# Kernel optimization log

Hardware: AMD Instinct MI355X
Metric: run time of the kernel (lower is better)

Reference implementation:

```python
import jax, jax.numpy as jnp
import numpy as np
from jax import lax


def _norm(a):
    a = np.asarray(a, np.float32)
    return a / (np.sqrt((a ** 2).sum()) + 1e-12)


LO = {
    'db4': _norm([-0.0105974017850021, 0.0328830116668852, 0.0308413818355607, -0.1870348117188811,
                  -0.0279837694169839, 0.6308807679295904, 0.7148465705529155, 0.2303778133088964]),
    'db6': _norm([0.00107730108499558, -0.00477725751101065, -0.0005538422009938, 0.03158203931748603,
                  0.02752286553030533, -0.0975016055873225, -0.12976686756709563, 0.22626469396544,
                  0.3152503517092432, -0.7511339080210959, 0.4946238903984534, 0.1115407433501095]),
    'sym6': _norm([-0.007800708325034148, 0.001767711864242804, 0.04472490177066578, -0.02106029251230056,
                   -0.0726375227866, 0.3379294217282401, 0.787641141030194, 0.4910559419267466,
                   -0.048311742585632, -0.1179901111484105, 0.00349071208421747, 0.01540410932702737]),
    'coif5': _norm([-3.459977283621256e-05, -7.098330313814114e-05, 0.0004662169601128863, 0.001117518770890601,
                    -0.002574517688750223, -0.00900797613666158, 0.015880544863615904, 0.03455502757306163,
                    -0.08230192710688598, -0.07179982161931202, 0.42848347637761874, 0.7937772226256206,
                    0.4051769024096169, -0.06112339000267287, -0.06577191128185562, 0.023452696141836267,
                    0.007782596427325418, -0.003793512864491014, -0.0002606761356811993, 0.000107502882505652,
                    1.10319778524429e-05, -5.520763127949e-06, -1.0682196848076e-06, 5.236425333584e-07,
                    1.125098976034e-07, -5.417490769329e-08, -8.8631e-09, 4.2921e-09, 6.7e-10, -3.2e-10]),
}
FIR_NAMES = ['db4', 'db6', 'sym6', 'coif5']
LIFT97 = (-1.586134342, -0.05298011854, 0.8829110762, 0.4435068522)


def _neighbor_sum(y):
    # 0.5*(y[i-1]+y[i+1]) with reflect padding on last axis
    yp = jnp.pad(y, [(0, 0)] * (y.ndim - 1) + [(1, 1)], mode='reflect')
    return 0.5 * (yp[..., :-2] + yp[..., 2:])


def _lift(xf, steps, sA, sD):
    # xf: [N, C]; even/odd split along signal axis, then predict/update lifting steps
    even, odd = xf[:, 0::2], xf[:, 1::2]
    for coeff, is_predict in steps:
        if is_predict:
            odd = odd + coeff * _neighbor_sum(even)
        else:
            even = even + coeff * _neighbor_sum(odd)
    return sA * even, sD * odd


def _fir(xf, lo_np):
    # xf: [N, C]; QMF analysis pair, reflect-padded 'same-ish' correlation (Lout = C-2 for even L)
    L = lo_np.shape[0]
    n = np.arange(L)
    hi_np = ((-1.0) ** n).astype(np.float32) * lo_np[::-1]
    pad = (L - 1) // 2
    pl, pr = (pad - 1, pad) if L % 2 == 0 else (pad, pad)
    xp = jnp.pad(xf[:, None, :], ((0, 0), (0, 0), (pl, pr)), mode='reflect')
    rhs = jnp.asarray(np.stack([lo_np, hi_np])[:, None, :])  # [2,1,L]
    out = lax.conv_general_dilated(xp, rhs, (1,), 'VALID', dimension_numbers=('NCH', 'OIH', 'NCH'))
    return out[:, 0], out[:, 1]


def _resize_linear(x, out_size):
    # matches torch F.interpolate(mode='linear', align_corners=False) on last axis
    Lin = x.shape[-1]
    if Lin == out_size:
        return x
    src = (np.arange(out_size) + 0.5) * (Lin / out_size) - 0.5
    src = np.clip(src, 0.0, None)
    i0 = np.minimum(np.floor(src).astype(np.int32), Lin - 1)
    i1 = np.minimum(i0 + 1, Lin - 1)
    w = jnp.asarray((src - i0).astype(np.float32))
    return x[..., i0] * (1.0 - w) + x[..., i1] * w


def setup_inputs() -> dict:
    key = jax.random.key(0)
    ks = jax.random.split(key, 4)
    B, C, H, W, O, K = 8, 64, 128, 128, 64, 6
    G = max(4, int(C * 0.25))
    return {
        'x': jax.random.normal(ks[0], (B, C, H, W), jnp.float32),
        'gate_w1': jax.random.normal(ks[1], (G, C), jnp.float32) * 0.1,
        'gate_b1': jnp.zeros((G,), jnp.float32),
        'gate_w2': jax.random.normal(ks[2], (K, G), jnp.float32) * 0.1,
        'gate_b2': jnp.zeros((K,), jnp.float32),
        'proj_w': jax.random.normal(ks[3], (O, 2 * C), jnp.float32) * 0.05,
        'proj_b': jnp.zeros((O,), jnp.float32),
        'scale53_A': jnp.asarray(1.0, jnp.float32),
        'scale53_D': jnp.asarray(1.0, jnp.float32),
        'scale97_A': jnp.asarray(1.149604398, jnp.float32),
        'scale97_D': jnp.asarray(1.0 / 1.149604398, jnp.float32),
    }


def reference(x, gate_w1, gate_b1, gate_w2, gate_b2, proj_w, proj_b,
              scale53_A, scale53_D, scale97_A, scale97_D):
    B, C, H, W = x.shape
    # per-pixel gate over K candidates (two 1x1 convs + softmax)
    h = jax.nn.relu(jnp.einsum('bchw,gc->bghw', x, gate_w1) + gate_b1[None, :, None, None])
    logits = jnp.einsum('bghw,kg->bkhw', h, gate_w2) + gate_b2[None, :, None, None]
    gate = jax.nn.softmax(logits, axis=1)

    xf = x.transpose(0, 2, 3, 1).reshape(B * H * W, C)  # signal axis = channels
    As, Ds = [], []
    for name in FIR_NAMES:
        A, D = _fir(xf, LO[name])
        As.append(_resize_linear(A, C))
        Ds.append(_resize_linear(D, C))
    A, D = _lift(xf, [(-0.5, True), (0.25, False)], scale53_A, scale53_D)
    As.append(_resize_linear(A, C)); Ds.append(_resize_linear(D, C))
    al, be, ga, de = LIFT97
    A, D = _lift(xf, [(al, True), (be, False), (ga, True), (de, False)], scale97_A, scale97_D)
    As.append(_resize_linear(A, C)); Ds.append(_resize_linear(D, C))

    A_cat = jnp.stack(As, axis=1)  # [BHW, K, C]
    D_cat = jnp.stack(Ds, axis=1)
    wm = gate.transpose(0, 2, 3, 1).reshape(B * H * W, -1)
    wm = wm / (wm.sum(axis=1, keepdims=True) + 1e-12)
    A_f = jnp.einsum('nkc,nk->nc', A_cat, wm)
    D_f = jnp.einsum('nkc,nk->nc', D_cat, wm)

    Y = jnp.concatenate([A_f, D_f], axis=1).reshape(B, H, W, 2 * C)
    out = jnp.einsum('bhwc,oc->bohw', Y, proj_w) + proj_b[None, :, None, None]
    return out
```

## Files before the change

### kernel.cpp

```cpp
#include <hip/hip_runtime.h>
#include <hip/hip_bf16.h>
#include <math.h>

typedef __bf16 bf16x4 __attribute__((ext_vector_type(4)));
typedef __bf16 bf16x8 __attribute__((ext_vector_type(8)));
typedef float  f32x4  __attribute__((ext_vector_type(4)));

#define HW 16384
#define CCH 64
#define OCH 64

__device__ static const float FIRTAB[62] = {
  -0.0105974017850021f, 0.0328830116668852f, 0.0308413818355607f, -0.1870348117188811f,
  -0.0279837694169839f, 0.6308807679295904f, 0.7148465705529155f, 0.2303778133088964f,
  0.00107730108499558f, -0.00477725751101065f, -0.0005538422009938f, 0.03158203931748603f,
  0.02752286553030533f, -0.0975016055873225f, -0.12976686756709563f, 0.22626469396544f,
  0.3152503517092432f, -0.7511339080210959f, 0.4946238903984534f, 0.1115407433501095f,
  -0.007800708325034148f, 0.001767711864242804f, 0.04472490177066578f, -0.02106029251230056f,
  -0.0726375227866f, 0.3379294217282401f, 0.787641141030194f, 0.4910559419267466f,
  -0.048311742585632f, -0.1179901111484105f, 0.00349071208421747f, 0.01540410932702737f,
  -3.459977283621256e-05f, -7.098330313814114e-05f, 0.0004662169601128863f, 0.001117518770890601f,
  -0.002574517688750223f, -0.00900797613666158f, 0.015880544863615904f, 0.03455502757306163f,
  -0.08230192710688598f, -0.07179982161931202f, 0.42848347637761874f, 0.7937772226256206f,
  0.4051769024096169f, -0.06112339000267287f, -0.06577191128185562f, 0.023452696141836267f,
  0.007782596427325418f, -0.003793512864491014f, -0.0002606761356811993f, 0.000107502882505652f,
  1.10319778524429e-05f, -5.520763127949e-06f, -1.0682196848076e-06f, 5.236425333584e-07f,
  1.125098976034e-07f, -5.417490769329e-08f, -8.8631e-09f, 4.2921e-09f, 6.7e-10f, -3.2e-10f
};
__device__ static const int FIR_OFF[4] = {0, 8, 20, 32};
__device__ static const int FIR_LEN[4] = {8, 12, 12, 30};

__global__ __launch_bounds__(256) void setup_P(
    const float* __restrict__ pw,
    const float* __restrict__ s53A, const float* __restrict__ s53D,
    const float* __restrict__ s97A, const float* __restrict__ s97D,
    __bf16* __restrict__ Pout)
{
  __shared__ float tmpA[62][64];
  __shared__ float tmpD[62][64];
  __shared__ float matA[64][64];
  __shared__ float matD[64][64];
  __shared__ float pwld[8][128];
  __shared__ float rawS[32], loS[32], hiS[32];

  const int k = blockIdx.x >> 3;
  const int q = blockIdx.x & 7;
  const int t = threadIdx.x;

  {
    const float* src = pw + q * 8 * 128;
    #pragma unroll
    for (int i = 0; i < 4; ++i)
      ((float*)pwld)[t + i * 256] = src[t + i * 256];
  }

  if (k < 4) {
    const int L = FIR_LEN[k], off = FIR_OFF[k];
    const int pl = (L - 1) / 2 - 1;

    if (t < L) rawS[t] = FIRTAB[off + t];
    __syncthreads();
    float ss = 0.f;
    for (int l = 0; l < L; ++l) { float vv = rawS[l]; ss += vv * vv; }
    const float inv = 1.f / (sqrtf(ss) + 1e-12f);
    if (t < L) {
      loS[t] = rawS[t] * inv;
      hiS[t] = ((t & 1) ? -1.f : 1.f) * rawS[L - 1 - t] * inv;
    }
    __syncthreads();

    for (int e = t; e < 62 * 64; e += 256) {
      const int i = e >> 6, c = e & 63;
      const int base = pl - i;
      const int l1 = c + base;
      const int l2 = -c + base;
      const int l3 = 126 - c + base;
      float va = 0.f, vd = 0.f;
      if (l1 >= 0 && l1 < L)           { va += loS[l1]; vd += hiS[l1]; }
      if (c > 0 && l2 >= 0 && l2 < L)  { va += loS[l2]; vd += hiS[l2]; }
      if (c < 63 && l3 >= 0 && l3 < L) { va += loS[l3]; vd += hiS[l3]; }
      tmpA[i][c] = va; tmpD[i][c] = vd;
    }
    __syncthreads();
  } else {
    for (int e = t; e < 32 * 64; e += 256) {
      const int i = e >> 6, c = e & 63;
      tmpA[i][c] = (c == 2 * i)     ? 1.f : 0.f;
      tmpD[i][c] = (c == 2 * i + 1) ? 1.f : 0.f;
    }
    float cf[4]; int nst;
    if (k == 4) { cf[0] = -0.5f; cf[1] = 0.25f; cf[2] = 0.f; cf[3] = 0.f; nst = 2; }
    else { cf[0] = -1.586134342f; cf[1] = -0.05298011854f;
           cf[2] = 0.8829110762f; cf[3] = 0.4435068522f; nst = 4; }
    __syncthreads();
    for (int s = 0; s < nst; ++s) {
      for (int e = t; e < 32 * 64; e += 256) {
        const int i = e >> 6, c = e & 63;
        const int im = (i == 0) ? 1 : i - 1;
        const int ip = (i == 31) ? 30 : i + 1;
        if ((s & 1) == 0)
          tmpD[i][c] += cf[s] * 0.5f * (tmpA[im][c] + tmpA[ip][c]);
        else
          tmpA[i][c] += cf[s] * 0.5f * (tmpD[im][c] + tmpD[ip][c]);
      }
      __syncthreads();
    }
  }

  {
    const int Lin = (k < 4) ? 62 : 32;
    float sA = 1.f, sD = 1.f;
    if (k == 4) { sA = s53A[0]; sD = s53D[0]; }
    if (k == 5) { sA = s97A[0]; sD = s97D[0]; }
    const float step = (float)Lin / 64.0f;
    for (int e = t; e < 64 * 64; e += 256) {
      const int o = e >> 6, c = e & 63;
      float src = (o + 0.5f) * step - 0.5f;
      src = fmaxf(src, 0.f);
      int i0 = (int)floorf(src); if (i0 > Lin - 1) i0 = Lin - 1;
      int i1 = i0 + 1;           if (i1 > Lin - 1) i1 = Lin - 1;
      float w = src - (float)i0;
      matA[o][c] = sA * ((1.f - w) * tmpA[i0][c] + w * tmpA[i1][c]);
      matD[o][c] = sD * ((1.f - w) * tmpD[i0][c] + w * tmpD[i1][c]);
    }
  }
  __syncthreads();

  {
    const int oo = t >> 5;
    const int o  = q * 8 + oo;
    const int c0 = (t & 31) * 2;
    float acc0 = 0.f, acc1 = 0.f;
    #pragma unroll 8
    for (int j = 0; j < 64; ++j) {
      const float wa = pwld[oo][j];
      const float wd = pwld[oo][64 + j];
      acc0 += wa * matA[j][c0]     + wd * matD[j][c0];
      acc1 += wa * matA[j][c0 + 1] + wd * matD[j][c0 + 1];
    }
    const int mf = o >> 4;
    #pragma unroll
    for (int cc = 0; cc < 2; ++cc) {
      const int c = c0 + cc;
      const int s = k * 2 + (c >> 5);
      const int lane = (o & 15) | (((c & 31) >> 3) << 4);
      const int e = c & 7;
      Pout[(((s * 4 + mf) * 64 + lane) << 3) + e] = (__bf16)(cc ? acc1 : acc0);
    }
  }
}

__global__ __launch_bounds__(256, 2) void wavelet_main(
    const float* __restrict__ xg,
    const float* __restrict__ gw1, const float* __restrict__ gb1,
    const float* __restrict__ gw2, const float* __restrict__ gb2,
    const float* __restrict__ pbias,
    const __bf16* __restrict__ Pws,
    float* __restrict__ outg)
{
  __shared__ __align__(16) unsigned char xt[256 * 128];
  __shared__ __align__(16) float wmld[256 * 8];

  const int t    = threadIdx.x;
  const int w    = t >> 6;
  const int lane = t & 63;
  const int lr   = lane & 15;
  const int kq   = lane >> 4;

  const int blk   = blockIdx.x;
  const int b     = blk >> 6;
  const int pbase = (blk & 63) << 8;

  const int pq  = lane & 15;
  const int cg  = lane >> 4;
  const int px0 = w * 64 + pq * 4;

  const float* s = xg + (size_t)b * (CCH * HW) + (size_t)(cg * 16) * HW + pbase + px0;
  f32x4 v[16];
  #pragma unroll
  for (int r = 0; r < 16; ++r) v[r] = *(const f32x4*)(s + (size_t)r * HW);

  bf16x8 A[12];
  #pragma unroll
  for (int kk = 0; kk < 6; ++kk)
    #pragma unroll
    for (int sh = 0; sh < 2; ++sh)
      A[kk * 2 + sh] = *(const bf16x8*)(Pws + (size_t)((((2 * kk + sh) * 4 + w) * 64 + lane) << 3));

  bf16x8 W1a[2];
  {
    const float* wp = gw1 + lr * 64 + kq * 8;
    #pragma unroll
    for (int hh = 0; hh < 2; ++hh) {
      f32x4 lo = *(const f32x4*)(wp + hh * 32);
      f32x4 hi = *(const f32x4*)(wp + hh * 32 + 4);
      bf16x8 a;
      #pragma unroll
      for (int e = 0; e < 4; ++e) { a[e] = (__bf16)lo[e]; a[e + 4] = (__bf16)hi[e]; }
      W1a[hh] = a;
    }
  }
  const f32x4 gb1v  = *(const f32x4*)(gb1 + kq * 4);
  const f32x4 biasv = *(const f32x4*)(pbias + w * 16 + kq * 4);

  #pragma unroll
  for (int i = 0; i < 4; ++i) {
    const int px = px0 + i;
    bf16x8 w0, w1;
    #pragma unroll
    for (int e = 0; e < 8; ++e) { w0[e] = (__bf16)v[e][i]; w1[e] = (__bf16)v[8 + e][i]; }
    *(bf16x8*)&xt[px * 128 + (((cg * 2)     ^ (px & 7)) << 4)] = w0;
    *(bf16x8*)&xt[px * 128 + (((cg * 2 + 1) ^ (px & 7)) << 4)] = w1;
  }

  #pragma unroll
  for (int pp = 0; pp < 4; ++pp) {
    const int col = (w * 4 + pp) * 16 + lr;
    const bf16x8 B0 = *(const bf16x8*)&xt[col * 128 + ((kq       ^ (col & 7)) << 4)];
    const bf16x8 B1 = *(const bf16x8*)&xt[col * 128 + (((4 + kq) ^ (col & 7)) << 4)];

    f32x4 h = {0.f, 0.f, 0.f, 0.f};
    h = __builtin_amdgcn_mfma_f32_16x16x32_bf16(W1a[0], B0, h, 0, 0, 0);
    h = __builtin_amdgcn_mfma_f32_16x16x32_bf16(W1a[1], B1, h, 0, 0, 0);
    float hr[4];
    #pragma unroll
    for (int j = 0; j < 4; ++j) hr[j] = fmaxf(h[j] + gb1v[j], 0.f);

    float lg[6];
    #pragma unroll
    for (int kk = 0; kk < 6; ++kk) {
      const f32x4 w2 = *(const f32x4*)(gw2 + kk * 16 + kq * 4);
      lg[kk] = w2[0] * hr[0] + w2[1] * hr[1] + w2[2] * hr[2] + w2[3] * hr[3];
    }
    #pragma unroll
    for (int kk = 0; kk < 6; ++kk) lg[kk] += __shfl_xor(lg[kk], 16);
    #pragma unroll
    for (int kk = 0; kk < 6; ++kk) lg[kk] += __shfl_xor(lg[kk], 32);
    #pragma unroll
    for (int kk = 0; kk < 6; ++kk) lg[kk] += gb2[kk];

    float mx = fmaxf(fmaxf(fmaxf(lg[0], lg[1]), fmaxf(lg[2], lg[3])), fmaxf(lg[4], lg[5]));
    float ex[6], ssum = 0.f;
    #pragma unroll
    for (int kk = 0; kk < 6; ++kk) { ex[kk] = __expf(lg[kk] - mx); ssum += ex[kk]; }
    const float sinv = __builtin_amdgcn_rcpf(ssum);
    if (kq == 0) {
      f32x4 o0 = { ex[0] * sinv, ex[1] * sinv, ex[2] * sinv, ex[3] * sinv };
      f32x4 o1 = { ex[4] * sinv, ex[5] * sinv, 0.f, 0.f };
      *(f32x4*)&wmld[col * 8 + 0] = o0;
      *(f32x4*)&wmld[col * 8 + 4] = o1;
    }
  }
  __syncthreads();

  float* outb = outg + (size_t)b * (OCH * HW) + pbase;

  #pragma unroll
  for (int pg = 0; pg < 16; ++pg) {
    const int col = pg * 16 + lr;
    const bf16x8 B0 = *(const bf16x8*)&xt[col * 128 + ((kq       ^ (col & 7)) << 4)];
    const bf16x8 B1 = *(const bf16x8*)&xt[col * 128 + (((4 + kq) ^ (col & 7)) << 4)];
    const f32x4 wv0 = *(const f32x4*)&wmld[col * 8 + 0];
    const f32x4 wv1 = *(const f32x4*)&wmld[col * 8 + 4];
    const float wmv[6] = { wv0[0], wv0[1], wv0[2], wv0[3], wv1[0], wv1[1] };

    f32x4 facc = biasv;
    #pragma unroll
    for (int kk = 0; kk < 6; ++kk) {
      f32x4 y = {0.f, 0.f, 0.f, 0.f};
      y = __builtin_amdgcn_mfma_f32_16x16x32_bf16(A[2 * kk    ], B0, y, 0, 0, 0);
      y = __builtin_amdgcn_mfma_f32_16x16x32_bf16(A[2 * kk + 1], B1, y, 0, 0, 0);
      #pragma unroll
      for (int j = 0; j < 4; ++j) facc[j] += wmv[kk] * y[j];
    }
    #pragma unroll
    for (int j = 0; j < 4; ++j) {
      const int o = w * 16 + kq * 4 + j;
      __builtin_nontemporal_store(facc[j], &outb[(size_t)o * HW + col]);
    }
  }
}

extern "C" void kernel_launch(void* const* d_in, const int* in_sizes, int n_in,
                              void* d_out, int out_size, void* d_ws, size_t ws_size,
                              hipStream_t stream) {
  const float* x    = (const float*)d_in[0];
  const float* gw1  = (const float*)d_in[1];
  const float* gb1  = (const float*)d_in[2];
  const float* gw2  = (const float*)d_in[3];
  const float* gb2  = (const float*)d_in[4];
  const float* pw   = (const float*)d_in[5];
  const float* pb   = (const float*)d_in[6];
  const float* s53A = (const float*)d_in[7];
  const float* s53D = (const float*)d_in[8];
  const float* s97A = (const float*)d_in[9];
  const float* s97D = (const float*)d_in[10];
  __bf16* Pws = (__bf16*)d_ws;
  float* out = (float*)d_out;

  setup_P<<<48, 256, 0, stream>>>(pw, s53A, s53D, s97A, s97D, Pws);
  wavelet_main<<<512, 256, 0, stream>>>(x, gw1, gb1, gw2, gb2, pb, Pws, out);
}
```

Before: 30.79 us.

## Fuse setup and main kernels into one cooperative kernel with grid sync

Merges the projection-matrix setup kernel and the main wavelet kernel into a single cooperative launch. The first 48 blocks build the bf16 projection table after issuing their input loads, then a grid-wide sync publishes it before the projection MFMAs. Shared memory is a union of both stages' buffers. This aims to remove the second launch and the serialization gap between the kernels, and to overlap setup with input loading and the gating computation. In exchange it adds a grid barrier, relies on all 512 blocks being co-resident, and delays 48 blocks with extra work; it falls back to the two-kernel path if the cooperative launch fails.

```diff
diff --git a/kernel.cpp b/kernel.cpp
--- a/kernel.cpp
+++ b/kernel.cpp
@@ -1,6 +1,9 @@
 #include <hip/hip_runtime.h>
 #include <hip/hip_bf16.h>
+#include <hip/hip_cooperative_groups.h>
 #include <math.h>
+
+namespace cg = cooperative_groups;
 
 typedef __bf16 bf16x4 __attribute__((ext_vector_type(4)));
 typedef __bf16 bf16x8 __attribute__((ext_vector_type(8)));
@@ -30,42 +33,46 @@
 __device__ static const int FIR_OFF[4] = {0, 8, 20, 32};
 __device__ static const int FIR_LEN[4] = {8, 12, 12, 30};
 
-__global__ __launch_bounds__(256) void setup_P(
+struct PS {
+  float tmpA[62][64];
+  float tmpD[62][64];
+  float matA[64][64];
+  float matD[64][64];
+  float pwld[8][128];
+  float rawS[32], loS[32], hiS[32];
+};
+struct MS {
+  unsigned char xt[256 * 128];
+  float wmld[256 * 8];
+};
+union SU { PS p; MS m; };
+
+__device__ __forceinline__ void build_P(
+    PS& S, int k, int q, int t,
     const float* __restrict__ pw,
     const float* __restrict__ s53A, const float* __restrict__ s53D,
     const float* __restrict__ s97A, const float* __restrict__ s97D,
     __bf16* __restrict__ Pout)
 {
-  __shared__ float tmpA[62][64];
-  __shared__ float tmpD[62][64];
-  __shared__ float matA[64][64];
-  __shared__ float matD[64][64];
-  __shared__ float pwld[8][128];
-  __shared__ float rawS[32], loS[32], hiS[32];
-
-  const int k = blockIdx.x >> 3;
-  const int q = blockIdx.x & 7;
-  const int t = threadIdx.x;
-
   {
     const float* src = pw + q * 8 * 128;
     #pragma unroll
     for (int i = 0; i < 4; ++i)
-      ((float*)pwld)[t + i * 256] = src[t + i * 256];
+      ((float*)S.pwld)[t + i * 256] = src[t + i * 256];
   }
 
   if (k < 4) {
     const int L = FIR_LEN[k], off = FIR_OFF[k];
     const int pl = (L - 1) / 2 - 1;
 
-    if (t < L) rawS[t] = FIRTAB[off + t];
+    if (t < L) S.rawS[t] = FIRTAB[off + t];
     __syncthreads();
     float ss = 0.f;
-    for (int l = 0; l < L; ++l) { float vv = rawS[l]; ss += vv * vv; }
+    for (int l = 0; l < L; ++l) { float vv = S.rawS[l]; ss += vv * vv; }
     const float inv = 1.f / (sqrtf(ss) + 1e-12f);
     if (t < L) {
-      loS[t] = rawS[t] * inv;
-      hiS[t] = ((t & 1) ? -1.f : 1.f) * rawS[L - 1 - t] * inv;
+      S.loS[t] = S.rawS[t] * inv;
+      S.hiS[t] = ((t & 1) ? -1.f : 1.f) * S.rawS[L - 1 - t] * inv;
     }
     __syncthreads();
 
@@ -76,17 +83,17 @@
       const int l2 = -c + base;
       const int l3 = 126 - c + base;
       float va = 0.f, vd = 0.f;
-      if (l1 >= 0 && l1 < L)           { va += loS[l1]; vd += hiS[l1]; }
-      if (c > 0 && l2 >= 0 && l2 < L)  { va += loS[l2]; vd += hiS[l2]; }
-      if (c < 63 && l3 >= 0 && l3 < L) { va += loS[l3]; vd += hiS[l3]; }
-      tmpA[i][c] = va; tmpD[i][c] = vd;
+      if (l1 >= 0 && l1 < L)           { va += S.loS[l1]; vd += S.hiS[l1]; }
+      if (c > 0 && l2 >= 0 && l2 < L)  { va += S.loS[l2]; vd += S.hiS[l2]; }
+      if (c < 63 && l3 >= 0 && l3 < L) { va += S.loS[l3]; vd += S.hiS[l3]; }
+      S.tmpA[i][c] = va; S.tmpD[i][c] = vd;
     }
     __syncthreads();
   } else {
     for (int e = t; e < 32 * 64; e += 256) {
       const int i = e >> 6, c = e & 63;
-      tmpA[i][c] = (c == 2 * i)     ? 1.f : 0.f;
-      tmpD[i][c] = (c == 2 * i + 1) ? 1.f : 0.f;
+      S.tmpA[i][c] = (c == 2 * i)     ? 1.f : 0.f;
+      S.tmpD[i][c] = (c == 2 * i + 1) ? 1.f : 0.f;
     }
     float cf[4]; int nst;
     if (k == 4) { cf[0] = -0.5f; cf[1] = 0.25f; cf[2] = 0.f; cf[3] = 0.f; nst = 2; }
@@ -99,9 +106,9 @@
         const int im = (i == 0) ? 1 : i - 1;
         const int ip = (i == 31) ? 30 : i + 1;
         if ((s & 1) == 0)
-          tmpD[i][c] += cf[s] * 0.5f * (tmpA[im][c] + tmpA[ip][c]);
+          S.tmpD[i][c] += cf[s] * 0.5f * (S.tmpA[im][c] + S.tmpA[ip][c]);
         else
-          tmpA[i][c] += cf[s] * 0.5f * (tmpD[im][c] + tmpD[ip][c]);
+          S.tmpA[i][c] += cf[s] * 0.5f * (S.tmpD[im][c] + S.tmpD[ip][c]);
       }
       __syncthreads();
     }
@@ -120,8 +127,8 @@
       int i0 = (int)floorf(src); if (i0 > Lin - 1) i0 = Lin - 1;
       int i1 = i0 + 1;           if (i1 > Lin - 1) i1 = Lin - 1;
       float w = src - (float)i0;
-      matA[o][c] = sA * ((1.f - w) * tmpA[i0][c] + w * tmpA[i1][c]);
-      matD[o][c] = sD * ((1.f - w) * tmpD[i0][c] + w * tmpD[i1][c]);
+      S.matA[o][c] = sA * ((1.f - w) * S.tmpA[i0][c] + w * S.tmpA[i1][c]);
+      S.matD[o][c] = sD * ((1.f - w) * S.tmpD[i0][c] + w * S.tmpD[i1][c]);
     }
   }
   __syncthreads();
@@ -133,10 +140,10 @@
     float acc0 = 0.f, acc1 = 0.f;
     #pragma unroll 8
     for (int j = 0; j < 64; ++j) {
-      const float wa = pwld[oo][j];
-      const float wd = pwld[oo][64 + j];
-      acc0 += wa * matA[j][c0]     + wd * matD[j][c0];
-      acc1 += wa * matA[j][c0 + 1] + wd * matD[j][c0 + 1];
+      const float wa = S.pwld[oo][j];
+      const float wd = S.pwld[oo][64 + j];
+      acc0 += wa * S.matA[j][c0]     + wd * S.matD[j][c0];
+      acc1 += wa * S.matA[j][c0 + 1] + wd * S.matD[j][c0 + 1];
     }
     const int mf = o >> 4;
     #pragma unroll
@@ -148,6 +155,154 @@
       Pout[(((s * 4 + mf) * 64 + lane) << 3) + e] = (__bf16)(cc ? acc1 : acc0);
     }
   }
+  __syncthreads();
+}
+
+__global__ __launch_bounds__(256, 2) void fused(
+    const float* __restrict__ xg,
+    const float* __restrict__ gw1, const float* __restrict__ gb1,
+    const float* __restrict__ gw2, const float* __restrict__ gb2,
+    const float* __restrict__ pw,  const float* __restrict__ pbias,
+    const float* __restrict__ s53A, const float* __restrict__ s53D,
+    const float* __restrict__ s97A, const float* __restrict__ s97D,
+    __bf16* __restrict__ Pws,
+    float* __restrict__ outg)
+{
+  __shared__ __align__(16) SU u;
+
+  const int t    = threadIdx.x;
+  const int w    = t >> 6;
+  const int lane = t & 63;
+  const int lr   = lane & 15;
+  const int kq   = lane >> 4;
+
+  const int blk   = blockIdx.x;
+  const int b     = blk >> 6;
+  const int pbase = (blk & 63) << 8;
+
+  const int pq  = lane & 15;
+  const int cg  = lane >> 4;
+  const int px0 = w * 64 + pq * 4;
+
+  const float* s = xg + (size_t)b * (CCH * HW) + (size_t)(cg * 16) * HW + pbase + px0;
+  f32x4 v[16];
+  #pragma unroll
+  for (int r = 0; r < 16; ++r) v[r] = *(const f32x4*)(s + (size_t)r * HW);
+
+  if (blk < 48)
+    build_P(u.p, blk >> 3, blk & 7, t, pw, s53A, s53D, s97A, s97D, Pws);
+
+  bf16x8 W1a[2];
+  {
+    const float* wp = gw1 + lr * 64 + kq * 8;
+    #pragma unroll
+    for (int hh = 0; hh < 2; ++hh) {
+      f32x4 lo = *(const f32x4*)(wp + hh * 32);
+      f32x4 hi = *(const f32x4*)(wp + hh * 32 + 4);
+      bf16x8 a;
+      #pragma unroll
+      for (int e = 0; e < 4; ++e) { a[e] = (__bf16)lo[e]; a[e + 4] = (__bf16)hi[e]; }
+      W1a[hh] = a;
+    }
+  }
+  const f32x4 gb1v  = *(const f32x4*)(gb1 + kq * 4);
+  const f32x4 biasv = *(const f32x4*)(pbias + w * 16 + kq * 4);
+
+  #pragma unroll
+  for (int i = 0; i < 4; ++i) {
+    const int px = px0 + i;
+    bf16x8 w0, w1;
+    #pragma unroll
+    for (int e = 0; e < 8; ++e) { w0[e] = (__bf16)v[e][i]; w1[e] = (__bf16)v[8 + e][i]; }
+    *(bf16x8*)&u.m.xt[px * 128 + (((cg * 2)     ^ (px & 7)) << 4)] = w0;
+    *(bf16x8*)&u.m.xt[px * 128 + (((cg * 2 + 1) ^ (px & 7)) << 4)] = w1;
+  }
+
+  #pragma unroll
+  for (int pp = 0; pp < 4; ++pp) {
+    const int col = (w * 4 + pp) * 16 + lr;
+    const bf16x8 B0 = *(const bf16x8*)&u.m.xt[col * 128 + ((kq       ^ (col & 7)) << 4)];
+    const bf16x8 B1 = *(const bf16x8*)&u.m.xt[col * 128 + (((4 + kq) ^ (col & 7)) << 4)];
+
+    f32x4 h = {0.f, 0.f, 0.f, 0.f};
+    h = __builtin_amdgcn_mfma_f32_16x16x32_bf16(W1a[0], B0, h, 0, 0, 0);
+    h = __builtin_amdgcn_mfma_f32_16x16x32_bf16(W1a[1], B1, h, 0, 0, 0);
+    float hr[4];
+    #pragma unroll
+    for (int j = 0; j < 4; ++j) hr[j] = fmaxf(h[j] + gb1v[j], 0.f);
+
+    float lg[6];
+    #pragma unroll
+    for (int kk = 0; kk < 6; ++kk) {
+      const f32x4 w2 = *(const f32x4*)(gw2 + kk * 16 + kq * 4);
+      lg[kk] = w2[0] * hr[0] + w2[1] * hr[1] + w2[2] * hr[2] + w2[3] * hr[3];
+    }
+    #pragma unroll
+    for (int kk = 0; kk < 6; ++kk) lg[kk] += __shfl_xor(lg[kk], 16);
+    #pragma unroll
+    for (int kk = 0; kk < 6; ++kk) lg[kk] += __shfl_xor(lg[kk], 32);
+    #pragma unroll
+    for (int kk = 0; kk < 6; ++kk) lg[kk] += gb2[kk];
+
+    float mx = fmaxf(fmaxf(fmaxf(lg[0], lg[1]), fmaxf(lg[2], lg[3])), fmaxf(lg[4], lg[5]));
+    float ex[6], ssum = 0.f;
+    #pragma unroll
+    for (int kk = 0; kk < 6; ++kk) { ex[kk] = __expf(lg[kk] - mx); ssum += ex[kk]; }
+    const float sinv = __builtin_amdgcn_rcpf(ssum);
+    if (kq == 0) {
+      f32x4 o0 = { ex[0] * sinv, ex[1] * sinv, ex[2] * sinv, ex[3] * sinv };
+      f32x4 o1 = { ex[4] * sinv, ex[5] * sinv, 0.f, 0.f };
+      *(f32x4*)&u.m.wmld[col * 8 + 0] = o0;
+      *(f32x4*)&u.m.wmld[col * 8 + 4] = o1;
+    }
+  }
+
+  cg::this_grid().sync();
+
+  bf16x8 A[12];
+  #pragma unroll
+  for (int kk = 0; kk < 6; ++kk)
+    #pragma unroll
+    for (int sh = 0; sh < 2; ++sh)
+      A[kk * 2 + sh] = *(const bf16x8*)(Pws + (size_t)((((2 * kk + sh) * 4 + w) * 64 + lane) << 3));
+
+  float* outb = outg + (size_t)b * (OCH * HW) + pbase;
+
+  #pragma unroll
+  for (int pg = 0; pg < 16; ++pg) {
+    const int col = pg * 16 + lr;
+    const bf16x8 B0 = *(const bf16x8*)&u.m.xt[col * 128 + ((kq       ^ (col & 7)) << 4)];
+    const bf16x8 B1 = *(const bf16x8*)&u.m.xt[col * 128 + (((4 + kq) ^ (col & 7)) << 4)];
+    const f32x4 wv0 = *(const f32x4*)&u.m.wmld[col * 8 + 0];
+    const f32x4 wv1 = *(const f32x4*)&u.m.wmld[col * 8 + 4];
+    const float wmv[6] = { wv0[0], wv0[1], wv0[2], wv0[3], wv1[0], wv1[1] };
+
+    f32x4 facc = biasv;
+    #pragma unroll
+    for (int kk = 0; kk < 6; ++kk) {
+      f32x4 y = {0.f, 0.f, 0.f, 0.f};
+      y = __builtin_amdgcn_mfma_f32_16x16x32_bf16(A[2 * kk    ], B0, y, 0, 0, 0);
+      y = __builtin_amdgcn_mfma_f32_16x16x32_bf16(A[2 * kk + 1], B1, y, 0, 0, 0);
+      #pragma unroll
+      for (int j = 0; j < 4; ++j) facc[j] += wmv[kk] * y[j];
+    }
+    #pragma unroll
+    for (int j = 0; j < 4; ++j) {
+      const int o = w * 16 + kq * 4 + j;
+      __builtin_nontemporal_store(facc[j], &outb[(size_t)o * HW + col]);
+    }
+  }
+}
+
+__global__ __launch_bounds__(256) void setup_P(
+    const float* __restrict__ pw,
+    const float* __restrict__ s53A, const float* __restrict__ s53D,
+    const float* __restrict__ s97A, const float* __restrict__ s97D,
+    __bf16* __restrict__ Pout)
+{
+  __shared__ __align__(16) PS S;
+  build_P(S, blockIdx.x >> 3, blockIdx.x & 7, threadIdx.x,
+          pw, s53A, s53D, s97A, s97D, Pout);
 }
 
 __global__ __launch_bounds__(256, 2) void wavelet_main(
@@ -158,8 +313,7 @@
     const __bf16* __restrict__ Pws,
     float* __restrict__ outg)
 {
-  __shared__ __align__(16) unsigned char xt[256 * 128];
-  __shared__ __align__(16) float wmld[256 * 8];
+  __shared__ __align__(16) MS m;
 
   const int t    = threadIdx.x;
   const int w    = t >> 6;
@@ -209,15 +363,15 @@
     bf16x8 w0, w1;
     #pragma unroll
     for (int e = 0; e < 8; ++e) { w0[e] = (__bf16)v[e][i]; w1[e] = (__bf16)v[8 + e][i]; }
-    *(bf16x8*)&xt[px * 128 + (((cg * 2)     ^ (px & 7)) << 4)] = w0;
-    *(bf16x8*)&xt[px * 128 + (((cg * 2 + 1) ^ (px & 7)) << 4)] = w1;
+    *(bf16x8*)&m.xt[px * 128 + (((cg * 2)     ^ (px & 7)) << 4)] = w0;
+    *(bf16x8*)&m.xt[px * 128 + (((cg * 2 + 1) ^ (px & 7)) << 4)] = w1;
   }
 
   #pragma unroll
   for (int pp = 0; pp < 4; ++pp) {
     const int col = (w * 4 + pp) * 16 + lr;
-    const bf16x8 B0 = *(const bf16x8*)&xt[col * 128 + ((kq       ^ (col & 7)) << 4)];
-    const bf16x8 B1 = *(const bf16x8*)&xt[col * 128 + (((4 + kq) ^ (col & 7)) << 4)];
+    const bf16x8 B0 = *(const bf16x8*)&m.xt[col * 128 + ((kq       ^ (col & 7)) << 4)];
+    const bf16x8 B1 = *(const bf16x8*)&m.xt[col * 128 + (((4 + kq) ^ (col & 7)) << 4)];
 
     f32x4 h = {0.f, 0.f, 0.f, 0.f};
     h = __builtin_amdgcn_mfma_f32_16x16x32_bf16(W1a[0], B0, h, 0, 0, 0);
@@ -247,8 +401,8 @@
     if (kq == 0) {
       f32x4 o0 = { ex[0] * sinv, ex[1] * sinv, ex[2] * sinv, ex[3] * sinv };
       f32x4 o1 = { ex[4] * sinv, ex[5] * sinv, 0.f, 0.f };
-      *(f32x4*)&wmld[col * 8 + 0] = o0;
-      *(f32x4*)&wmld[col * 8 + 4] = o1;
+      *(f32x4*)&m.wmld[col * 8 + 0] = o0;
+      *(f32x4*)&m.wmld[col * 8 + 4] = o1;
     }
   }
   __syncthreads();
@@ -258,10 +412,10 @@
   #pragma unroll
   for (int pg = 0; pg < 16; ++pg) {
     const int col = pg * 16 + lr;
-    const bf16x8 B0 = *(const bf16x8*)&xt[col * 128 + ((kq       ^ (col & 7)) << 4)];
-    const bf16x8 B1 = *(const bf16x8*)&xt[col * 128 + (((4 + kq) ^ (col & 7)) << 4)];
-    const f32x4 wv0 = *(const f32x4*)&wmld[col * 8 + 0];
-    const f32x4 wv1 = *(const f32x4*)&wmld[col * 8 + 4];
+    const bf16x8 B0 = *(const bf16x8*)&m.xt[col * 128 + ((kq       ^ (col & 7)) << 4)];
+    const bf16x8 B1 = *(const bf16x8*)&m.xt[col * 128 + (((4 + kq) ^ (col & 7)) << 4)];
+    const f32x4 wv0 = *(const f32x4*)&m.wmld[col * 8 + 0];
+    const f32x4 wv1 = *(const f32x4*)&m.wmld[col * 8 + 4];
     const float wmv[6] = { wv0[0], wv0[1], wv0[2], wv0[3], wv1[0], wv1[1] };
 
     f32x4 facc = biasv;
@@ -298,6 +452,15 @@
   __bf16* Pws = (__bf16*)d_ws;
   float* out = (float*)d_out;
 
-  setup_P<<<48, 256, 0, stream>>>(pw, s53A, s53D, s97A, s97D, Pws);
-  wavelet_main<<<512, 256, 0, stream>>>(x, gw1, gb1, gw2, gb2, pb, Pws, out);
+  void* kargs[] = {
+    (void*)&x, (void*)&gw1, (void*)&gb1, (void*)&gw2, (void*)&gb2,
+    (void*)&pw, (void*)&pb, (void*)&s53A, (void*)&s53D, (void*)&s97A,
+    (void*)&s97D, (void*)&Pws, (void*)&out
+  };
+  hipError_t err = hipLaunchCooperativeKernel(
+      (const void*)fused, dim3(512), dim3(256), kargs, 0, stream);
+  if (err != hipSuccess) {
+    setup_P<<<48, 256, 0, stream>>>(pw, s53A, s53D, s97A, s97D, Pws);
+    wavelet_main<<<512, 256, 0, stream>>>(x, gw1, gb1, gw2, gb2, pb, Pws, out);
+  }
 }
```

Result: slower. 89.64 us (+191.2%).
